# Performance work log

Hardware: AMD Instinct MI355X
Metric: run time of the kernel (lower is better)

## Reference

```python
import jax, jax.numpy as jnp
import numpy as np

B, V, P, L, D = 8, 16, 128, 16, 128
PD = L * D  # patch_dim = patch_size * d_model = 2048


def _layernorm(x, g, b, eps=1e-5):
    mu = jnp.mean(x, axis=-1, keepdims=True)
    var = jnp.mean(jnp.square(x - mu), axis=-1, keepdims=True)
    return (x - mu) / jnp.sqrt(var + eps) * g + b


def setup_inputs() -> dict:
    key = jax.random.key(0)
    ks = jax.random.split(key, 24)
    x = jax.random.normal(ks[0], (B, V, P, L, D), jnp.float32)
    m = jax.random.randint(ks[1], (B, V, V), 0, 2) > 0
    var_mask = m & ~jnp.eye(V, dtype=bool)[None]  # keep self-attention unmasked

    def lin_w(k, fan_in, fan_out):
        return jax.random.normal(k, (fan_in, fan_out), jnp.float32) * (1.0 / np.sqrt(fan_in))

    inp = {"x": x, "var_mask": var_mask}
    # Attn_PatchLevel (attn1): query / shared kv / out projections
    inp["w_q1"] = lin_w(ks[2], PD, PD); inp["b_q1"] = jnp.zeros((PD,), jnp.float32)
    inp["w_kv1"] = lin_w(ks[3], PD, PD); inp["b_kv1"] = jnp.zeros((PD,), jnp.float32)
    inp["w_o1"] = lin_w(ks[4], PD, PD); inp["b_o1"] = jnp.zeros((PD,), jnp.float32)
    # Attn_VarLevel (attn2)
    inp["w_q2"] = lin_w(ks[5], PD, PD); inp["b_q2"] = jnp.zeros((PD,), jnp.float32)
    inp["w_kv2"] = lin_w(ks[6], PD, PD); inp["b_kv2"] = jnp.zeros((PD,), jnp.float32)
    inp["w_o2"] = lin_w(ks[7], PD, PD); inp["b_o2"] = jnp.zeros((PD,), jnp.float32)
    # LayerNorms
    inp["g1"] = jnp.ones((PD,), jnp.float32); inp["be1"] = jnp.zeros((PD,), jnp.float32)
    inp["g2"] = jnp.ones((PD,), jnp.float32); inp["be2"] = jnp.zeros((PD,), jnp.float32)
    inp["g3"] = jnp.ones((PD,), jnp.float32); inp["be3"] = jnp.zeros((PD,), jnp.float32)
    # FFN
    inp["w_l1"] = lin_w(ks[8], PD, 4 * PD); inp["b_l1"] = jnp.zeros((4 * PD,), jnp.float32)
    inp["w_l2"] = lin_w(ks[9], 4 * PD, PD); inp["b_l2"] = jnp.zeros((PD,), jnp.float32)
    return inp


def reference(x, var_mask,
              w_q1, b_q1, w_kv1, b_kv1, w_o1, b_o1,
              w_q2, b_q2, w_kv2, b_kv2, w_o2, b_o2,
              g1, be1, g2, be2, g3, be3,
              w_l1, b_l1, w_l2, b_l2):
    b, v, p, l, d = x.shape
    pd = l * d
    scale = 1.0 / np.sqrt(pd)
    x = x.reshape(b, v, p, pd)

    # ---- Attn_PatchLevel (mask=None -> no masking; keys and values share kv_projection) ----
    q = x @ w_q1 + b_q1
    kv = x @ w_kv1 + b_kv1  # keys == values in the original module
    scores = jnp.einsum('bvpd,bvsd->bvps', q, kv)  # [B,V,P,P]
    attn = jax.nn.softmax(scale * scores, axis=-1)  # dropout is identity at eval
    a1 = jnp.einsum('bvps,bvsd->bvpd', attn, kv) @ w_o1 + b_o1
    x = _layernorm(x + a1, g1, be1)

    # ---- Attn_VarLevel over variables, per patch ----
    x = x.transpose(0, 2, 1, 3)  # [B,P,V,PD]
    q = x @ w_q2 + b_q2
    kv = x @ w_kv2 + b_kv2
    scores = jnp.einsum('bpvd,bprd->bpvr', q, kv)  # [B,P,V,V]
    scores = jnp.where(var_mask[:, None, :, :], -jnp.inf, scores)
    attn = jax.nn.softmax(scale * scores, axis=-1)
    a2 = jnp.einsum('bpvr,bprd->bpvd', attn, kv) @ w_o2 + b_o2
    x = _layernorm(x + a2, g2, be2)

    # ---- FFN (torch nn.GELU default = exact erf) ----
    z = jax.nn.gelu(x @ w_l1 + b_l1, approximate=False)
    x = x + z @ w_l2 + b_l2

    x_out = _layernorm(x, g3, be3).transpose(0, 2, 1, 3)  # [B,V,P,PD]
    x_next = x_out.reshape(b, v, p // 2, 2 * l, d)
    return x_out, x_next
```

## Files before the change

kernel.cpp:

```cpp
#include <hip/hip_runtime.h>
#include <math.h>


using u16   = unsigned short;
using f32x4 = __attribute__((ext_vector_type(4))) float;
using bf16x8= __attribute__((ext_vector_type(8))) __bf16;
using u16x8 = __attribute__((ext_vector_type(8))) u16;
using u16x4 = __attribute__((ext_vector_type(4))) u16;

#define NROWS 16384
#define PD    2048
#define MEMBAR asm volatile("" ::: "memory")

__device__ __forceinline__ float bf2f(u16 u) {
    unsigned v = ((unsigned)u) << 16;
    return __builtin_bit_cast(float, v);
}
__device__ __forceinline__ u16 f2bf(float f) {
    unsigned u = __builtin_bit_cast(unsigned, f);
    u += 0x7FFFu + ((u >> 16) & 1u);
    return (u16)(u >> 16);
}
__device__ __forceinline__ void gload_lds16(const void* g, void* l) {
    __builtin_amdgcn_global_load_lds((const __attribute__((address_space(1))) void*)g,
                                     (__attribute__((address_space(3))) void*)l, 16, 0, 0);
}
__device__ __forceinline__ void block_barrier() {
    MEMBAR; __builtin_amdgcn_s_barrier(); MEMBAR;
}

template<int GELU>
__global__ __launch_bounds__(512, 2)
void gemm256(const u16* __restrict__ A, int lda,
             const u16* __restrict__ B, int ldb,
             u16* __restrict__ C, int ldc,
             const float* __restrict__ bias, int K,
             int NT, int CM, int CN)
{
    __shared__ __align__(16) char smem[131072];

    const int tid  = threadIdx.x;
    const int wv   = tid >> 6;
    const int wm   = wv >> 2;
    const int wn   = wv & 3;
    const int lane = tid & 63;
    const int fr   = lane & 15;
    const int fks16= (lane >> 4) * 16;
    const int rmask= (fr & 7) << 4;
    const int kb0  = fks16 ^ rmask;
    const int kb1  = (64 + fks16) ^ rmask;

    const int xcd = blockIdx.x & 7;
    const int ii  = blockIdx.x >> 3;
    const int RY  = NT / CN;
    const int mt  = (xcd / RY) * CM + (ii / CN);
    const int nt  = (xcd % RY) * CN + (ii % CN);
    const int m0  = mt * 256;
    const int n0  = nt * 256;

    const int rsub = tid >> 3;
    const int cswE = (((tid & 7) * 16) ^ ((rsub & 7) << 4)) >> 1;
    const int waveByte = wv * 1024;

    auto stage = [&](const u16* mat, int ld, int row0, int k0, int regionByte) {
        const u16* g0 = mat + (size_t)(row0 + rsub) * ld + k0 + cswE;
        gload_lds16(g0,                   smem + regionByte + waveByte);
        gload_lds16(g0 + (size_t)ld * 64, smem + regionByte + 8192 + waveByte);
    };

    const int aRowByte = (wm * 128 + fr) * 128;
    const int bRowByte = (wn * 64 + fr) * 128;

    const int KT = K >> 6;

    stage(A, lda, m0,       0, 0);
    stage(B, ldb, n0,       0, 32768);
    stage(A, lda, m0 + 128, 0, 16384);
    stage(B, ldb, n0 + 128, 0, 49152);
    stage(B, ldb, n0,      64, 98304);
    stage(A, lda, m0,      64, 65536);
    asm volatile("s_waitcnt vmcnt(4)" ::: "memory");
    block_barrier();

    bf16x8 a[4][2], b0[2][2], b1[2][2];
    f32x4  acc[8][4] = {};

    for (int t = 0; t < KT; ++t) {
        const int Ab = (t & 1) ? 65536 : 0;
        const int Bb = Ab + 32768;
        const int Ob = Ab ^ 65536;
        const bool s1 = (t + 1 < KT), s2 = (t + 2 < KT);

        #pragma unroll
        for (int mi = 0; mi < 4; ++mi) {
            const int rb = Ab + aRowByte + mi * 2048;
            a[mi][0] = *(const bf16x8*)(smem + rb + kb0);
            a[mi][1] = *(const bf16x8*)(smem + rb + kb1);
        }
        #pragma unroll
        for (int nj = 0; nj < 2; ++nj) {
            const int rb = Bb + bRowByte + nj * 2048;
            b0[nj][0] = *(const bf16x8*)(smem + rb + kb0);
            b0[nj][1] = *(const bf16x8*)(smem + rb + kb1);
        }
        if (s1) stage(B, ldb, n0 + 128, (t + 1) << 6, Ob + 49152);
        __builtin_amdgcn_s_setprio(1);
        #pragma unroll
        for (int mi = 0; mi < 4; ++mi)
            #pragma unroll
            for (int nj = 0; nj < 2; ++nj) {
                acc[mi][nj] = __builtin_amdgcn_mfma_f32_16x16x32_bf16(a[mi][0], b0[nj][0], acc[mi][nj], 0, 0, 0);
                acc[mi][nj] = __builtin_amdgcn_mfma_f32_16x16x32_bf16(a[mi][1], b0[nj][1], acc[mi][nj], 0, 0, 0);
            }
        __builtin_amdgcn_s_setprio(0);
        block_barrier();

        #pragma unroll
        for (int nj = 0; nj < 2; ++nj) {
            const int rb = Bb + bRowByte + 4096 + nj * 2048;
            b1[nj][0] = *(const bf16x8*)(smem + rb + kb0);
            b1[nj][1] = *(const bf16x8*)(smem + rb + kb1);
        }
        if (s1) stage(A, lda, m0 + 128, (t + 1) << 6, Ob + 16384);
        __builtin_amdgcn_s_setprio(1);
        #pragma unroll
        for (int mi = 0; mi < 4; ++mi)
            #pragma unroll
            for (int nj = 0; nj < 2; ++nj) {
                acc[mi][2 + nj] = __builtin_amdgcn_mfma_f32_16x16x32_bf16(a[mi][0], b1[nj][0], acc[mi][2 + nj], 0, 0, 0);
                acc[mi][2 + nj] = __builtin_amdgcn_mfma_f32_16x16x32_bf16(a[mi][1], b1[nj][1], acc[mi][2 + nj], 0, 0, 0);
            }
        __builtin_amdgcn_s_setprio(0);
        block_barrier();

        #pragma unroll
        for (int mi = 0; mi < 4; ++mi) {
            const int rb = Ab + aRowByte + 8192 + mi * 2048;
            a[mi][0] = *(const bf16x8*)(smem + rb + kb0);
            a[mi][1] = *(const bf16x8*)(smem + rb + kb1);
        }
        if (s2) stage(B, ldb, n0, (t + 2) << 6, Bb);
        __builtin_amdgcn_s_setprio(1);
        #pragma unroll
        for (int mi = 0; mi < 4; ++mi)
            #pragma unroll
            for (int nj = 0; nj < 2; ++nj) {
                acc[4 + mi][nj] = __builtin_amdgcn_mfma_f32_16x16x32_bf16(a[mi][0], b0[nj][0], acc[4 + mi][nj], 0, 0, 0);
                acc[4 + mi][nj] = __builtin_amdgcn_mfma_f32_16x16x32_bf16(a[mi][1], b0[nj][1], acc[4 + mi][nj], 0, 0, 0);
            }
        __builtin_amdgcn_s_setprio(0);
        block_barrier();

        if (s2) stage(A, lda, m0, (t + 2) << 6, Ab);
        __builtin_amdgcn_s_setprio(1);
        #pragma unroll
        for (int mi = 0; mi < 4; ++mi)
            #pragma unroll
            for (int nj = 0; nj < 2; ++nj) {
                acc[4 + mi][2 + nj] = __builtin_amdgcn_mfma_f32_16x16x32_bf16(a[mi][0], b1[nj][0], acc[4 + mi][2 + nj], 0, 0, 0);
                acc[4 + mi][2 + nj] = __builtin_amdgcn_mfma_f32_16x16x32_bf16(a[mi][1], b1[nj][1], acc[4 + mi][2 + nj], 0, 0, 0);
            }
        __builtin_amdgcn_s_setprio(0);
        if (s2) { asm volatile("s_waitcnt vmcnt(4)" ::: "memory"); }
        else    { asm volatile("s_waitcnt vmcnt(0)" ::: "memory"); }
        block_barrier();
    }

    u16* lsu = (u16*)smem;
    const int lcol = wn * 64 + fr;
    const int lrow = wm * 128 + (lane >> 4) * 4;
    #pragma unroll
    for (int nj = 0; nj < 4; ++nj) {
        const float bb = bias[n0 + lcol + nj * 16];
        #pragma unroll
        for (int mi = 0; mi < 8; ++mi) {
            #pragma unroll
            for (int j = 0; j < 4; ++j) {
                float v = acc[mi][nj][j] + bb;
                if constexpr (GELU) v = 0.5f * v * (1.f + erff(v * 0.70710678118f));
                lsu[(lrow + mi * 16 + j) * 256 + lcol + nj * 16] = f2bf(v);
            }
        }
    }
    block_barrier();
    const int hp = tid & 31;
    const int r0 = tid >> 5;
    #pragma unroll
    for (int ps = 0; ps < 16; ++ps) {
        const int r = ps * 16 + r0;
        u16x8 v = *(const u16x8*)&lsu[r * 256 + hp * 8];
        *(u16x8*)&C[(size_t)(m0 + r) * ldc + n0 + hp * 8] = v;
    }
}

template<int OUTF32, int HASBIAS>
__global__ __launch_bounds__(256, 2)
void gemm_nt(const u16* __restrict__ A, long sAg, int lda,
             const u16* __restrict__ B, long sBg, int ldb,
             void* __restrict__ Cv, long sCg, int ldc,
             const float* __restrict__ bias, int K, float scale)
{
    __shared__ __align__(16) u16 lsA[128 * 32];
    __shared__ __align__(16) u16 lsB[128 * 32];

    const int tid  = threadIdx.x;
    const int w    = tid >> 6;
    const int lane = tid & 63;
    const int m0   = blockIdx.x * 128;
    const int n0   = blockIdx.y * 128;
    A += (long)blockIdx.z * sAg;
    B += (long)blockIdx.z * sBg;

    const int wr = w >> 1, wc = w & 1;
    f32x4 acc[4][4] = {};

    const int srow = lane >> 2;
    const int skc  = (lane & 3) * 8;
    const int rA0  = 32 * w + srow;
    const int rA1  = rA0 + 16;
    const size_t aoff0 = (size_t)(m0 + rA0) * lda + skc;
    const size_t aoff1 = (size_t)(m0 + rA1) * lda + skc;
    const size_t boff0 = (size_t)(n0 + rA0) * ldb + skc;
    const size_t boff1 = (size_t)(n0 + rA1) * ldb + skc;
    u16* lA0 = lsA + 1024 * w;
    u16* lA1 = lA0 + 512;
    u16* lB0 = lsB + 1024 * w;
    u16* lB1 = lB0 + 512;

    const int fr = lane & 15;
    const int fk = (lane >> 4) * 8;

    for (int k0 = 0; k0 < K; k0 += 32) {
        gload_lds16(A + aoff0 + k0, lA0);
        gload_lds16(A + aoff1 + k0, lA1);
        gload_lds16(B + boff0 + k0, lB0);
        gload_lds16(B + boff1 + k0, lB1);
        __syncthreads();

        bf16x8 af[4], bf[4];
        #pragma unroll
        for (int m = 0; m < 4; m++)
            af[m] = *(const bf16x8*)&lsA[(wr * 64 + m * 16 + fr) * 32 + fk];
        #pragma unroll
        for (int n = 0; n < 4; n++)
            bf[n] = *(const bf16x8*)&lsB[(wc * 64 + n * 16 + fr) * 32 + fk];
        #pragma unroll
        for (int m = 0; m < 4; m++)
            #pragma unroll
            for (int n = 0; n < 4; n++)
                acc[m][n] = __builtin_amdgcn_mfma_f32_16x16x32_bf16(af[m], bf[n], acc[m][n], 0, 0, 0);
        __syncthreads();
    }

    float* Cf = (float*)Cv;
    u16*   Cb = (u16*)Cv;
    const int crow0 = m0 + wr * 64 + (lane >> 4) * 4;
    const int ccol0 = n0 + wc * 64 + fr;
    const long cbase = (long)blockIdx.z * sCg;
    #pragma unroll
    for (int n = 0; n < 4; n++) {
        const int col = ccol0 + n * 16;
        float bb = 0.f;
        if constexpr (HASBIAS) bb = bias[col];
        #pragma unroll
        for (int m = 0; m < 4; m++) {
            #pragma unroll
            for (int j = 0; j < 4; j++) {
                const int row = crow0 + m * 16 + j;
                float v = acc[m][n][j] + bb;
                const long idx = cbase + (long)row * ldc + col;
                if constexpr (OUTF32) Cf[idx] = v * scale;
                else                  Cb[idx] = f2bf(v);
            }
        }
    }
}

__global__ __launch_bounds__(256)
void wtrans_kernel(const float* __restrict__ in, u16* __restrict__ out, int R, int C)
{
    __shared__ float tile[32][33];
    const int c0 = blockIdx.x * 32, r0 = blockIdx.y * 32;
    const int tx = threadIdx.x & 31, ty = threadIdx.x >> 5;
    #pragma unroll
    for (int i = ty; i < 32; i += 8)
        tile[i][tx] = in[(size_t)(r0 + i) * C + c0 + tx];
    __syncthreads();
    #pragma unroll
    for (int i = ty; i < 32; i += 8)
        out[(size_t)(c0 + i) * R + r0 + tx] = f2bf(tile[tx][i]);
}

__global__ __launch_bounds__(256)
void kvtrans_kernel(const u16* __restrict__ in, u16* __restrict__ out)
{
    __shared__ u16 tile[32][33];
    const int g = blockIdx.z;
    const int n0 = blockIdx.x * 32, m0 = blockIdx.y * 32;
    const int tx = threadIdx.x & 31, ty = threadIdx.x >> 5;
    #pragma unroll
    for (int i = ty; i < 32; i += 8)
        tile[i][tx] = in[(size_t)(g * 128 + m0 + i) * 2048 + n0 + tx];
    __syncthreads();
    #pragma unroll
    for (int i = ty; i < 32; i += 8)
        out[(size_t)g * 262144 + (size_t)(n0 + i) * 128 + m0 + tx] = tile[tx][i];
}

__global__ __launch_bounds__(256)
void cvt_f32_bf16(const float* __restrict__ in, u16* __restrict__ out)
{
    const long i = ((long)blockIdx.x * 256 + threadIdx.x) * 4;
    float4 v = *(const float4*)(in + i);
    u16x4 o;
    o[0] = f2bf(v.x); o[1] = f2bf(v.y); o[2] = f2bf(v.z); o[3] = f2bf(v.w);
    *(u16x4*)(out + i) = o;
}

template<int FINAL>
__global__ __launch_bounds__(256)
void ln_kernel(const float* __restrict__ resid, const u16* __restrict__ add,
               const float* __restrict__ gam, const float* __restrict__ bet,
               u16* __restrict__ xb, float* __restrict__ o1, float* __restrict__ o2)
{
    const long row = blockIdx.x;
    const int  t   = threadIdx.x;
    const long base = row * PD + t * 8;

    u16x8  av = *(const u16x8*)(add + base);
    float4 r0 = *(const float4*)(resid + base);
    float4 r1 = *(const float4*)(resid + base + 4);
    float y[8];
    y[0] = r0.x + bf2f(av[0]); y[1] = r0.y + bf2f(av[1]);
    y[2] = r0.z + bf2f(av[2]); y[3] = r0.w + bf2f(av[3]);
    y[4] = r1.x + bf2f(av[4]); y[5] = r1.y + bf2f(av[5]);
    y[6] = r1.z + bf2f(av[6]); y[7] = r1.w + bf2f(av[7]);

    float s1 = 0.f, s2 = 0.f;
    #pragma unroll
    for (int j = 0; j < 8; j++) { s1 += y[j]; s2 += y[j] * y[j]; }
    #pragma unroll
    for (int d = 1; d < 64; d <<= 1) { s1 += __shfl_xor(s1, d); s2 += __shfl_xor(s2, d); }
    __shared__ float red[8];
    const int w = t >> 6;
    if ((t & 63) == 0) { red[w] = s1; red[4 + w] = s2; }
    __syncthreads();
    s1 = red[0] + red[1] + red[2] + red[3];
    s2 = red[4] + red[5] + red[6] + red[7];
    const float mean = s1 * (1.f / PD);
    const float var  = s2 * (1.f / PD) - mean * mean;
    const float rstd = rsqrtf(var + 1e-5f);

    float4 g0 = *(const float4*)(gam + t * 8);
    float4 g1 = *(const float4*)(gam + t * 8 + 4);
    float4 b0 = *(const float4*)(bet + t * 8);
    float4 b1 = *(const float4*)(bet + t * 8 + 4);
    float gv[8] = {g0.x, g0.y, g0.z, g0.w, g1.x, g1.y, g1.z, g1.w};
    float bv[8] = {b0.x, b0.y, b0.z, b0.w, b1.x, b1.y, b1.z, b1.w};

    float o[8];
    #pragma unroll
    for (int j = 0; j < 8; j++) o[j] = (y[j] - mean) * rstd * gv[j] + bv[j];

    if constexpr (FINAL) {
        float4 p0 = {o[0], o[1], o[2], o[3]}, p1 = {o[4], o[5], o[6], o[7]};
        *(float4*)(o1 + base) = p0; *(float4*)(o1 + base + 4) = p1;
        *(float4*)(o2 + base) = p0; *(float4*)(o2 + base + 4) = p1;
    } else {
        u16x8 ob;
        #pragma unroll
        for (int j = 0; j < 8; j++) ob[j] = f2bf(o[j]);
        *(u16x8*)(xb + base) = ob;
        float4 p0 = {o[0], o[1], o[2], o[3]}, p1 = {o[4], o[5], o[6], o[7]};
        *(float4*)(o1 + base) = p0; *(float4*)(o1 + base + 4) = p1;
    }
}

__global__ __launch_bounds__(256)
void softmax128_kernel(const float* __restrict__ S, u16* __restrict__ P)
{
    const int row  = blockIdx.x * 4 + (threadIdx.x >> 6);
    const int lane = threadIdx.x & 63;
    const float2 v = *(const float2*)(S + (size_t)row * 128 + lane * 2);
    float mx = fmaxf(v.x, v.y);
    #pragma unroll
    for (int d = 1; d < 64; d <<= 1) mx = fmaxf(mx, __shfl_xor(mx, d));
    const float e0 = __expf(v.x - mx), e1 = __expf(v.y - mx);
    float sm = e0 + e1;
    #pragma unroll
    for (int d = 1; d < 64; d <<= 1) sm += __shfl_xor(sm, d);
    const float inv = 1.f / sm;
    unsigned o = (unsigned)f2bf(e0 * inv) | ((unsigned)f2bf(e1 * inv) << 16);
    *(unsigned*)(P + (size_t)row * 128 + lane * 2) = o;
}

__global__ void detect_mask_kernel(const unsigned char* __restrict__ m, int* __restrict__ flag)
{
    __shared__ int s;
    if (threadIdx.x == 0) s = 0;
    __syncthreads();
    int acc = 0;
    for (int i = threadIdx.x; i < 2048; i += 256)
        if (i & 3) acc |= m[i];
    if (acc) atomicOr(&s, 1);
    __syncthreads();
    if (threadIdx.x == 0) *flag = s;
}

__global__ __launch_bounds__(64)
void attn2_kernel(u16* __restrict__ Q, const u16* __restrict__ KV,
                  const void* __restrict__ mask, const int* __restrict__ mflag,
                  float scale)
{
    const int g = blockIdx.x;
    const int b = g >> 7, p = g & 127;
    const int lane = threadIdx.x;

    const size_t groupbase = ((size_t)(b * 16) * 128 + p) * PD;
    const size_t vstride   = (size_t)128 * PD;

    const int am   = lane & 15;
    const int koff = (lane >> 4) * 8;
    const u16* qp = Q  + groupbase + (size_t)am * vstride + koff;
    const u16* kp = KV + groupbase + (size_t)am * vstride + koff;

    f32x4 acc = {0.f, 0.f, 0.f, 0.f};
    for (int k0 = 0; k0 < PD; k0 += 32) {
        bf16x8 a  = *(const bf16x8*)(qp + k0);
        bf16x8 bb = *(const bf16x8*)(kp + k0);
        acc = __builtin_amdgcn_mfma_f32_16x16x32_bf16(a, bb, acc, 0, 0, 0);
    }

    const int vk = lane & 15;
    const int hi = lane >> 4;
    const int mf = *mflag;
    __shared__ float PL[16][16];
    float pv[4];
    #pragma unroll
    for (int j = 0; j < 4; j++) {
        const int vq = hi * 4 + j;
        float s = acc[j] * scale;
        const int midx = b * 256 + vq * 16 + vk;
        int msk;
        if (mf) msk = ((const unsigned char*)mask)[midx];
        else    msk = ((const int*)mask)[midx];
        if (msk) s = -1e30f;
        pv[j] = s;
    }
    #pragma unroll
    for (int j = 0; j < 4; j++) {
        float mx = pv[j];
        #pragma unroll
        for (int d = 1; d < 16; d <<= 1) mx = fmaxf(mx, __shfl_xor(mx, d));
        const float e = __expf(pv[j] - mx);
        float sm = e;
        #pragma unroll
        for (int d = 1; d < 16; d <<= 1) sm += __shfl_xor(sm, d);
        pv[j] = e / sm;
    }
    #pragma unroll
    for (int j = 0; j < 4; j++) PL[hi * 4 + j][vk] = pv[j];
    __syncthreads();

    const u16* kvr[16];
    #pragma unroll
    for (int v = 0; v < 16; v++) kvr[v] = KV + groupbase + (size_t)v * vstride;

    for (int vqt = 0; vqt < 16; vqt += 4) {
        float pr[4][16];
        #pragma unroll
        for (int q = 0; q < 4; q++)
            #pragma unroll
            for (int k = 0; k < 16; k++) pr[q][k] = PL[vqt + q][k];
        u16* o0 = Q + groupbase + (size_t)(vqt + 0) * vstride;
        u16* o1 = Q + groupbase + (size_t)(vqt + 1) * vstride;
        u16* o2 = Q + groupbase + (size_t)(vqt + 2) * vstride;
        u16* o3 = Q + groupbase + (size_t)(vqt + 3) * vstride;
        for (int n0 = 0; n0 < PD; n0 += 64) {
            const int n = n0 + lane;
            float a0 = 0.f, a1 = 0.f, a2 = 0.f, a3 = 0.f;
            #pragma unroll
            for (int k = 0; k < 16; k++) {
                const float kvv = bf2f(kvr[k][n]);
                a0 += pr[0][k] * kvv; a1 += pr[1][k] * kvv;
                a2 += pr[2][k] * kvv; a3 += pr[3][k] * kvv;
            }
            o0[n] = f2bf(a0); o1[n] = f2bf(a1); o2[n] = f2bf(a2); o3[n] = f2bf(a3);
        }
    }
}

extern "C" void kernel_launch(void* const* d_in, const int* in_sizes, int n_in,
                              void* d_out, int out_size, void* d_ws, size_t ws_size,
                              hipStream_t stream)
{
    const float* x0    = (const float*)d_in[0];
    const void*  vmask = d_in[1];
    const float* w_q1  = (const float*)d_in[2];  const float* b_q1  = (const float*)d_in[3];
    const float* w_kv1 = (const float*)d_in[4];  const float* b_kv1 = (const float*)d_in[5];
    const float* w_o1  = (const float*)d_in[6];  const float* b_o1  = (const float*)d_in[7];
    const float* w_q2  = (const float*)d_in[8];  const float* b_q2  = (const float*)d_in[9];
    const float* w_kv2 = (const float*)d_in[10]; const float* b_kv2 = (const float*)d_in[11];
    const float* w_o2  = (const float*)d_in[12]; const float* b_o2  = (const float*)d_in[13];
    const float* g1 = (const float*)d_in[14]; const float* be1 = (const float*)d_in[15];
    const float* g2 = (const float*)d_in[16]; const float* be2 = (const float*)d_in[17];
    const float* g3 = (const float*)d_in[18]; const float* be3 = (const float*)d_in[19];
    const float* w_l1 = (const float*)d_in[20]; const float* b_l1 = (const float*)d_in[21];
    const float* w_l2 = (const float*)d_in[22]; const float* b_l2 = (const float*)d_in[23];

    char* ws = (char*)d_ws;
    size_t off = 0;
    auto alloc = [&](size_t bytes) { size_t o = off; off += (bytes + 255) & ~(size_t)255; return o; };
    const size_t oWQ1  = alloc(8388608),  oWKV1 = alloc(8388608),  oWO1 = alloc(8388608);
    const size_t oWQ2  = alloc(8388608),  oWKV2 = alloc(8388608),  oWO2 = alloc(8388608);
    const size_t oWL1  = alloc(33554432), oWL2  = alloc(33554432);
    const size_t oXB   = alloc(67108864);
    const size_t oQ    = alloc(67108864);
    const size_t oKV   = alloc(67108864);
    const size_t oKVT  = alloc(67108864);
    const size_t oR    = alloc(134217728);
    const size_t oS    = alloc(8388608);
    const size_t oP1   = alloc(4194304);
    const size_t oFLAG = alloc(256);
    if (ws_size < off) return;

    u16* WQ1T = (u16*)(ws + oWQ1);  u16* WKV1T = (u16*)(ws + oWKV1); u16* WO1T = (u16*)(ws + oWO1);
    u16* WQ2T = (u16*)(ws + oWQ2);  u16* WKV2T = (u16*)(ws + oWKV2); u16* WO2T = (u16*)(ws + oWO2);
    u16* WL1T = (u16*)(ws + oWL1);  u16* WL2T  = (u16*)(ws + oWL2);
    u16* XB   = (u16*)(ws + oXB);   u16* Q     = (u16*)(ws + oQ);
    u16* KV   = (u16*)(ws + oKV);   u16* KVT   = (u16*)(ws + oKVT);
    float* R  = (float*)(ws + oR);  float* S   = (float*)(ws + oS);
    u16* P1   = (u16*)(ws + oP1);   int* FLAG  = (int*)(ws + oFLAG);
    u16* H    = Q;
    u16* F    = KVT;

    const float scale = 0.02209708691f;
    float* out0 = (float*)d_out;
    float* out1 = out0 + (size_t)NROWS * PD;

    detect_mask_kernel<<<1, 256, 0, stream>>>((const unsigned char*)vmask, FLAG);

    wtrans_kernel<<<dim3(64, 64), 256, 0, stream>>>(w_q1,  WQ1T,  2048, 2048);
    wtrans_kernel<<<dim3(64, 64), 256, 0, stream>>>(w_kv1, WKV1T, 2048, 2048);
    wtrans_kernel<<<dim3(64, 64), 256, 0, stream>>>(w_o1,  WO1T,  2048, 2048);
    wtrans_kernel<<<dim3(64, 64), 256, 0, stream>>>(w_q2,  WQ2T,  2048, 2048);
    wtrans_kernel<<<dim3(64, 64), 256, 0, stream>>>(w_kv2, WKV2T, 2048, 2048);
    wtrans_kernel<<<dim3(64, 64), 256, 0, stream>>>(w_o2,  WO2T,  2048, 2048);
    wtrans_kernel<<<dim3(256, 64), 256, 0, stream>>>(w_l1, WL1T, 2048, 8192);
    wtrans_kernel<<<dim3(64, 256), 256, 0, stream>>>(w_l2, WL2T, 8192, 2048);

    cvt_f32_bf16<<<32768, 256, 0, stream>>>(x0, XB);


    gemm256<0><<<512, 512, 0, stream>>>(XB, 2048, WQ1T,  2048, Q,  2048, b_q1,  2048, 8, 32, 2);
    gemm256<0><<<512, 512, 0, stream>>>(XB, 2048, WKV1T, 2048, KV, 2048, b_kv1, 2048, 8, 32, 2);
    kvtrans_kernel<<<dim3(64, 4, 128), 256, 0, stream>>>(KV, KVT);
    gemm_nt<1,0><<<dim3(1,1,128), 256, 0, stream>>>(Q, 262144, 2048, KV, 262144, 2048, S, 16384, 128, nullptr, 2048, scale);
    softmax128_kernel<<<4096, 256, 0, stream>>>(S, P1);
    gemm_nt<0,0><<<dim3(1,16,128), 256, 0, stream>>>(P1, 16384, 128, KVT, 262144, 128, Q, 262144, 2048, nullptr, 128, 1.f);
    gemm256<0><<<512, 512, 0, stream>>>(Q, 2048, WO1T, 2048, KV, 2048, b_o1, 2048, 8, 32, 2);
    ln_kernel<0><<<NROWS, 256, 0, stream>>>(x0, KV, g1, be1, XB, R, nullptr);

    gemm256<0><<<512, 512, 0, stream>>>(XB, 2048, WQ2T,  2048, Q,  2048, b_q2,  2048, 8, 32, 2);
    gemm256<0><<<512, 512, 0, stream>>>(XB, 2048, WKV2T, 2048, KV, 2048, b_kv2, 2048, 8, 32, 2);
    attn2_kernel<<<1024, 64, 0, stream>>>(Q, KV, vmask, FLAG, scale);
    gemm256<0><<<512, 512, 0, stream>>>(Q, 2048, WO2T, 2048, KV, 2048, b_o2, 2048, 8, 32, 2);
    ln_kernel<0><<<NROWS, 256, 0, stream>>>(R, KV, g2, be2, XB, R, nullptr);

    for (int c = 0; c < 2; c++) {
        const size_t rows = (size_t)c * 8192;
        for (int h = 0; h < 2; h++) {
            gemm256<1><<<512, 512, 0, stream>>>(XB + rows * 2048, 2048,
                                                WL1T + (size_t)h * 4096 * 2048, 2048,
                                                H + h * 4096, 8192,
                                                b_l1 + h * 4096, 2048, 16, 32, 2);
        }
        gemm256<0><<<256, 512, 0, stream>>>(H, 8192, WL2T, 8192, F + rows * 2048, 2048, b_l2, 8192, 8, 32, 1);
    }
    ln_kernel<1><<<NROWS, 256, 0, stream>>>(R, F, g3, be3, nullptr, out0, out1);
}
```

Baseline: 2.431 ms.

## Merge Q/KV projections into one GEMM launch and tighten LDS barrier scheduling

```diff
diff --git a/kernel.cpp b/kernel.cpp
--- a/kernel.cpp
+++ b/kernel.cpp
@@ -33,9 +33,9 @@
 __global__ __launch_bounds__(512, 2)
 void gemm256(const u16* __restrict__ A, int lda,
              const u16* __restrict__ B, int ldb,
-             u16* __restrict__ C, int ldc,
-             const float* __restrict__ bias, int K,
-             int NT, int CM, int CN)
+             u16* __restrict__ C1, u16* __restrict__ C2, int ncut, int ldc,
+             const float* __restrict__ bias1, const float* __restrict__ bias2,
+             int K, int NT, int CM, int CN)
 {
     __shared__ __align__(16) char smem[131072];
 
@@ -80,7 +80,7 @@
     stage(B, ldb, n0,      64, 98304);
     stage(A, lda, m0,      64, 65536);
     asm volatile("s_waitcnt vmcnt(4)" ::: "memory");
-    block_barrier();
+    __builtin_amdgcn_s_barrier();
 
     bf16x8 a[4][2], b0[2][2], b1[2][2];
     f32x4  acc[8][4] = {};
@@ -104,6 +104,9 @@
             b0[nj][1] = *(const bf16x8*)(smem + rb + kb1);
         }
         if (s1) stage(B, ldb, n0 + 128, (t + 1) << 6, Ob + 49152);
+        __builtin_amdgcn_s_barrier();
+        asm volatile("s_waitcnt lgkmcnt(0)" ::: "memory");
+        __builtin_amdgcn_sched_barrier(0);
         __builtin_amdgcn_s_setprio(1);
         #pragma unroll
         for (int mi = 0; mi < 4; ++mi)
@@ -113,7 +116,7 @@
                 acc[mi][nj] = __builtin_amdgcn_mfma_f32_16x16x32_bf16(a[mi][1], b0[nj][1], acc[mi][nj], 0, 0, 0);
             }
         __builtin_amdgcn_s_setprio(0);
-        block_barrier();
+        __builtin_amdgcn_s_barrier();
 
         #pragma unroll
         for (int nj = 0; nj < 2; ++nj) {
@@ -122,6 +125,9 @@
             b1[nj][1] = *(const bf16x8*)(smem + rb + kb1);
         }
         if (s1) stage(A, lda, m0 + 128, (t + 1) << 6, Ob + 16384);
+        __builtin_amdgcn_s_barrier();
+        asm volatile("s_waitcnt lgkmcnt(0)" ::: "memory");
+        __builtin_amdgcn_sched_barrier(0);
         __builtin_amdgcn_s_setprio(1);
         #pragma unroll
         for (int mi = 0; mi < 4; ++mi)
@@ -131,7 +137,7 @@
                 acc[mi][2 + nj] = __builtin_amdgcn_mfma_f32_16x16x32_bf16(a[mi][1], b1[nj][1], acc[mi][2 + nj], 0, 0, 0);
             }
         __builtin_amdgcn_s_setprio(0);
-        block_barrier();
+        __builtin_amdgcn_s_barrier();
 
         #pragma unroll
         for (int mi = 0; mi < 4; ++mi) {
@@ -140,6 +146,9 @@
             a[mi][1] = *(const bf16x8*)(smem + rb + kb1);
         }
         if (s2) stage(B, ldb, n0, (t + 2) << 6, Bb);
+        __builtin_amdgcn_s_barrier();
+        asm volatile("s_waitcnt lgkmcnt(0)" ::: "memory");
+        __builtin_amdgcn_sched_barrier(0);
         __builtin_amdgcn_s_setprio(1);
         #pragma unroll
         for (int mi = 0; mi < 4; ++mi)
@@ -149,9 +158,10 @@
                 acc[4 + mi][nj] = __builtin_amdgcn_mfma_f32_16x16x32_bf16(a[mi][1], b0[nj][1], acc[4 + mi][nj], 0, 0, 0);
             }
         __builtin_amdgcn_s_setprio(0);
-        block_barrier();
+        __builtin_amdgcn_s_barrier();
 
         if (s2) stage(A, lda, m0, (t + 2) << 6, Ab);
+        __builtin_amdgcn_s_barrier();
         __builtin_amdgcn_s_setprio(1);
         #pragma unroll
         for (int mi = 0; mi < 4; ++mi)
@@ -163,22 +173,28 @@
         __builtin_amdgcn_s_setprio(0);
         if (s2) { asm volatile("s_waitcnt vmcnt(4)" ::: "memory"); }
         else    { asm volatile("s_waitcnt vmcnt(0)" ::: "memory"); }
-        block_barrier();
-    }
-
+        __builtin_amdgcn_s_barrier();
+    }
+
+    u16* Cout; const float* bs; int ncol;
+    if (n0 < ncut) { Cout = C1; bs = bias1; ncol = n0; }
+    else           { Cout = C2; bs = bias2; ncol = n0 - ncut; }
+
+    block_barrier();
     u16* lsu = (u16*)smem;
-    const int lcol = wn * 64 + fr;
-    const int lrow = wm * 128 + (lane >> 4) * 4;
+    const int lcolB = wn * 64 + fr;
+    const int lrowB = wm * 128 + (lane >> 4) * 4;
     #pragma unroll
     for (int nj = 0; nj < 4; ++nj) {
-        const float bb = bias[n0 + lcol + nj * 16];
+        const int lcol = lcolB + nj * 16;
+        const float bb = bs[ncol + lcol];
         #pragma unroll
         for (int mi = 0; mi < 8; ++mi) {
             #pragma unroll
             for (int j = 0; j < 4; ++j) {
                 float v = acc[mi][nj][j] + bb;
                 if constexpr (GELU) v = 0.5f * v * (1.f + erff(v * 0.70710678118f));
-                lsu[(lrow + mi * 16 + j) * 256 + lcol + nj * 16] = f2bf(v);
+                lsu[(lrowB + mi * 16 + j) * 256 + lcol] = f2bf(v);
             }
         }
     }
@@ -189,7 +205,7 @@
     for (int ps = 0; ps < 16; ++ps) {
         const int r = ps * 16 + r0;
         u16x8 v = *(const u16x8*)&lsu[r * 256 + hp * 8];
-        *(u16x8*)&C[(size_t)(m0 + r) * ldc + n0 + hp * 8] = v;
+        *(u16x8*)&Cout[(size_t)(m0 + r) * ldc + ncol + hp * 8] = v;
     }
 }
 
@@ -551,31 +567,32 @@
 
     cvt_f32_bf16<<<32768, 256, 0, stream>>>(x0, XB);
 
-
-    gemm256<0><<<512, 512, 0, stream>>>(XB, 2048, WQ1T,  2048, Q,  2048, b_q1,  2048, 8, 32, 2);
-    gemm256<0><<<512, 512, 0, stream>>>(XB, 2048, WKV1T, 2048, KV, 2048, b_kv1, 2048, 8, 32, 2);
+    const int BIG = 1 << 30;
+
+    gemm256<0><<<1024, 512, 0, stream>>>(XB, 2048, WQ1T, 2048, Q, KV, 2048, 2048,
+                                         b_q1, b_kv1, 2048, 16, 32, 4);
     kvtrans_kernel<<<dim3(64, 4, 128), 256, 0, stream>>>(KV, KVT);
     gemm_nt<1,0><<<dim3(1,1,128), 256, 0, stream>>>(Q, 262144, 2048, KV, 262144, 2048, S, 16384, 128, nullptr, 2048, scale);
     softmax128_kernel<<<4096, 256, 0, stream>>>(S, P1);
     gemm_nt<0,0><<<dim3(1,16,128), 256, 0, stream>>>(P1, 16384, 128, KVT, 262144, 128, Q, 262144, 2048, nullptr, 128, 1.f);
-    gemm256<0><<<512, 512, 0, stream>>>(Q, 2048, WO1T, 2048, KV, 2048, b_o1, 2048, 8, 32, 2);
+    gemm256<0><<<512, 512, 0, stream>>>(Q, 2048, WO1T, 2048, KV, KV, BIG, 2048,
+                                        b_o1, b_o1, 2048, 8, 32, 2);
     ln_kernel<0><<<NROWS, 256, 0, stream>>>(x0, KV, g1, be1, XB, R, nullptr);
 
-    gemm256<0><<<512, 512, 0, stream>>>(XB, 2048, WQ2T,  2048, Q,  2048, b_q2,  2048, 8, 32, 2);
-    gemm256<0><<<512, 512, 0, stream>>>(XB, 2048, WKV2T, 2048, KV, 2048, b_kv2, 2048, 8, 32, 2);
+    gemm256<0><<<1024, 512, 0, stream>>>(XB, 2048, WQ2T, 2048, Q, KV, 2048, 2048,
+                                         b_q2, b_kv2, 2048, 16, 32, 4);
     attn2_kernel<<<1024, 64, 0, stream>>>(Q, KV, vmask, FLAG, scale);
-    gemm256<0><<<512, 512, 0, stream>>>(Q, 2048, WO2T, 2048, KV, 2048, b_o2, 2048, 8, 32, 2);
+    gemm256<0><<<512, 512, 0, stream>>>(Q, 2048, WO2T, 2048, KV, KV, BIG, 2048,
+                                        b_o2, b_o2, 2048, 8, 32, 2);
     ln_kernel<0><<<NROWS, 256, 0, stream>>>(R, KV, g2, be2, XB, R, nullptr);
 
     for (int c = 0; c < 2; c++) {
         const size_t rows = (size_t)c * 8192;
-        for (int h = 0; h < 2; h++) {
-            gemm256<1><<<512, 512, 0, stream>>>(XB + rows * 2048, 2048,
-                                                WL1T + (size_t)h * 4096 * 2048, 2048,
-                                                H + h * 4096, 8192,
-                                                b_l1 + h * 4096, 2048, 16, 32, 2);
-        }
-        gemm256<0><<<256, 512, 0, stream>>>(H, 8192, WL2T, 8192, F + rows * 2048, 2048, b_l2, 8192, 8, 32, 1);
+        gemm256<1><<<1024, 512, 0, stream>>>(XB + rows * 2048, 2048, WL1T, 2048,
+                                             H, H, BIG, 8192, b_l1, b_l1, 2048, 32, 32, 4);
+        gemm256<0><<<256, 512, 0, stream>>>(H, 8192, WL2T, 8192,
+                                            F + rows * 2048, F + rows * 2048, BIG, 2048,
+                                            b_l2, b_l2, 8192, 8, 32, 1);
     }
     ln_kernel<1><<<NROWS, 256, 0, stream>>>(R, F, g3, be3, nullptr, out0, out1);
 }
```

Result: no change. 2.474 ms (+1.8%).
